# Optimization experiments

Measured on AMD Instinct MI355X. Metric: run time of the kernel, lower is better.

The kernel has to match this reference:

```python
import jax, jax.numpy as jnp
import numpy as np

D_MODEL = 1024
H = 16
D_K = D_MODEL // H
NEG_INF = -1.0e9  # matches masked_fill value in the torch source


def setup_inputs() -> dict:
    key = jax.random.key(0)
    kq, kk, kv, kwq, kwk, kwv, kwo = jax.random.split(key, 7)
    B, S = 2, 2048
    query = jax.random.normal(kq, (B, S, D_MODEL), dtype=jnp.float32)
    key_t = jax.random.normal(kk, (B, S, D_MODEL), dtype=jnp.float32)
    value = jax.random.normal(kv, (B, S, D_MODEL), dtype=jnp.float32)
    # causal mask: 1 = attend, 0 = masked (masked_fill(mask == 0, -1e9))
    masked_val = jnp.tril(jnp.ones((S, S), dtype=jnp.int32))[None, None, :, :]
    scale = 1.0 / np.sqrt(D_MODEL)
    w_q = jax.random.normal(kwq, (D_MODEL, D_MODEL), dtype=jnp.float32) * scale
    w_k = jax.random.normal(kwk, (D_MODEL, D_MODEL), dtype=jnp.float32) * scale
    w_v = jax.random.normal(kwv, (D_MODEL, D_MODEL), dtype=jnp.float32) * scale
    w_o = jax.random.normal(kwo, (D_MODEL, D_MODEL), dtype=jnp.float32) * scale
    return {"query": query, "key": key_t, "value": value, "masked_val": masked_val,
            "w_q": w_q, "w_k": w_k, "w_v": w_v, "w_o": w_o}


def reference(query, key, value, masked_val, w_q, w_k, w_v, w_o):
    B, Sq, _ = query.shape
    Sk = key.shape[1]
    # nn.Linear(x) = x @ W.T; weights stored as [out, in]
    Q = (query @ w_q.T).reshape(B, Sq, H, D_K).transpose(0, 2, 1, 3)  # [B,H,Sq,Dk]
    K = (key @ w_k.T).reshape(B, Sk, H, D_K).transpose(0, 2, 1, 3)    # [B,H,Sk,Dk]
    V = (value @ w_v.T).reshape(B, Sk, H, D_K).transpose(0, 2, 1, 3)  # [B,H,Sk,Dk]
    scores = jnp.einsum("bhqd,bhkd->bhqk", Q, K) / jnp.sqrt(jnp.float32(D_K))
    scores = jnp.where(masked_val == 0, NEG_INF, scores)
    probs = jax.nn.softmax(scores, axis=-1)  # dropout p=0.0 -> identity
    ctx = jnp.einsum("bhqk,bhkd->bhqd", probs, V)  # [B,H,Sq,Dk]
    ctx = ctx.transpose(0, 2, 1, 3).reshape(B, Sq, H * D_K)
    return ctx @ w_o.T
```

## Files before the change

### kernel.cpp

```cpp
#include <hip/hip_runtime.h>
#include <hip/hip_bf16.h>
#include <type_traits>

using bf16x8_t = __attribute__((ext_vector_type(8))) __bf16;
using f32x4_t  = __attribute__((ext_vector_type(4))) float;

#define MFMA16(a, b, c) __builtin_amdgcn_mfma_f32_16x16x32_bf16((a), (b), (c), 0, 0, 0)

constexpr int BATCH   = 2;
constexpr int SEQ     = 2048;
constexpr int DMODEL  = 1024;
constexpr int DK      = 64;
constexpr int MTOT    = BATCH * SEQ;
constexpr float SCL2 = 0.125f * 1.44269504088896f;

typedef const __attribute__((address_space(1))) unsigned int ga_u32;
typedef __attribute__((address_space(3))) unsigned int ls_u32;
__device__ __forceinline__ void glds16(const void* g, void* l) {
    __builtin_amdgcn_global_load_lds((ga_u32*)g, (ls_u32*)l, 16, 0, 0);
}

__device__ __forceinline__ float exp2_fast(float x) {
    float r;
    asm volatile("v_exp_f32 %0, %1" : "=v"(r) : "v"(x));
    return r;
}

__device__ __forceinline__ bf16x8_t cvt8(const float* __restrict__ p) {
    f32x4_t a = *(const f32x4_t*)p;
    f32x4_t b = *(const f32x4_t*)(p + 4);
    bf16x8_t r;
    r[0] = (__bf16)a[0]; r[1] = (__bf16)a[1]; r[2] = (__bf16)a[2]; r[3] = (__bf16)a[3];
    r[4] = (__bf16)b[0]; r[5] = (__bf16)b[1]; r[6] = (__bf16)b[2]; r[7] = (__bf16)b[3];
    return r;
}

__global__ __launch_bounds__(256) void cvt_all_kernel(
    const float* __restrict__ q, const float* __restrict__ k, const float* __restrict__ v,
    const float* __restrict__ w0, const float* __restrict__ w1,
    const float* __restrict__ w2, const float* __restrict__ w3,
    __bf16* __restrict__ dstA, __bf16* __restrict__ dstW)
{
    const int y = blockIdx.y;
    const float* src;
    __bf16* dst;
    if (y < 3) {
        const float* a[3] = {q, k, v};
        src = a[y];
        dst = dstA + (size_t)y * (MTOT * DMODEL);
    } else {
        if (blockIdx.x >= 512) return;
        const float* w[4] = {w0, w1, w2, w3};
        src = w[y - 3];
        dst = dstW + (size_t)(y - 3) * (DMODEL * DMODEL);
    }
    size_t i = ((size_t)blockIdx.x * 256 + threadIdx.x) * 8;
    *(bf16x8_t*)(dst + i) = cvt8(src + i);
}

template<bool C_F32>
__device__ __forceinline__ void gemm_body(
    const __bf16* __restrict__ A, const __bf16* __restrict__ Bt,
    void* __restrict__ Cp, int m0, int n0, float cscale)
{
    constexpr int K = DMODEL, N = DMODEL;
    constexpr int NS = K / 32;
    __shared__ __align__(16) char smem[3][16384];

    const int tid  = threadIdx.x;
    const int wave = tid >> 6, lane = tid & 63;
    const int wm = wave >> 1, wn = wave & 1;
    const int l15 = lane & 15, lhi = lane >> 4;

    auto stage = [&](int k0, int buf) {
        #pragma unroll
        for (int i = 0; i < 2; ++i) {
            int cbase = i * 256 + wave * 64;
            int slot = cbase + lane;
            int row = slot >> 2, c = slot & 3;
            int cs = (c + 4 - ((row >> 1) & 3)) & 3;
            glds16(A + (size_t)(m0 + row) * K + k0 + cs * 8, smem[buf] + (size_t)cbase * 16);
        }
        #pragma unroll
        for (int i = 0; i < 2; ++i) {
            int cbase = i * 256 + wave * 64;
            int slot = cbase + lane;
            int row = slot >> 2, c = slot & 3;
            int cs = (c + 4 - ((row >> 1) & 3)) & 3;
            glds16(Bt + (size_t)(n0 + row) * K + k0 + cs * 8,
                   smem[buf] + 8192 + (size_t)cbase * 16);
        }
    };

    f32x4_t acc[4][4] = {};

    auto mfma_step = [&](int buf) {
        const __bf16* a_ls = (const __bf16*)smem[buf];
        const __bf16* b_ls = (const __bf16*)(smem[buf] + 8192);
        bf16x8_t af[4], bfr[4];
        #pragma unroll
        for (int i = 0; i < 4; ++i) {
            int row = wm * 64 + i * 16 + l15;
            int lc = (lhi + (row >> 1)) & 3;
            af[i] = *(const bf16x8_t*)(a_ls + row * 32 + lc * 8);
        }
        #pragma unroll
        for (int j = 0; j < 4; ++j) {
            int row = wn * 64 + j * 16 + l15;
            int lc = (lhi + (row >> 1)) & 3;
            bfr[j] = *(const bf16x8_t*)(b_ls + row * 32 + lc * 8);
        }
        #pragma unroll
        for (int i = 0; i < 4; ++i)
            #pragma unroll
            for (int j = 0; j < 4; ++j)
                acc[i][j] = MFMA16(af[i], bfr[j], acc[i][j]);
    };

    stage(0, 0);
    stage(32, 1);

    for (int t = 0; t < NS - 2; ++t) {
        asm volatile("s_waitcnt vmcnt(4)" ::: "memory");
        __builtin_amdgcn_s_barrier();
        __builtin_amdgcn_sched_barrier(0);
        stage((t + 2) * 32, (t + 2) % 3);
        mfma_step(t % 3);
    }
    asm volatile("s_waitcnt vmcnt(4)" ::: "memory");
    __builtin_amdgcn_s_barrier();
    __builtin_amdgcn_sched_barrier(0);
    mfma_step((NS - 2) % 3);
    asm volatile("s_waitcnt vmcnt(0)" ::: "memory");
    __builtin_amdgcn_s_barrier();
    __builtin_amdgcn_sched_barrier(0);
    mfma_step((NS - 1) % 3);

    #pragma unroll
    for (int i = 0; i < 4; ++i)
        #pragma unroll
        for (int j = 0; j < 4; ++j)
            #pragma unroll
            for (int r = 0; r < 4; ++r) {
                int row = m0 + wm * 64 + i * 16 + lhi * 4 + r;
                int col = n0 + wn * 64 + j * 16 + l15;
                float v = acc[i][j][r] * cscale;
                if constexpr (C_F32)
                    ((float*)Cp)[(size_t)row * N + col] = v;
                else
                    ((__bf16*)Cp)[(size_t)row * N + col] = (__bf16)v;
            }
}

__global__ __launch_bounds__(256) void proj_qkv_kernel(
    const __bf16* __restrict__ act, const __bf16* __restrict__ wc,
    __bf16* __restrict__ oq, __bf16* __restrict__ ok, __bf16* __restrict__ ov)
{
    int lid = blockIdx.x + 8 * blockIdx.y + 256 * blockIdx.z;
    int nid = (lid & 7) * 96 + (lid >> 3);
    int z = nid >> 8, rem = nid & 255;
    int m0 = (rem >> 3) * 128, n0 = (rem & 7) * 128;

    const __bf16* A = act + (size_t)z * (MTOT * DMODEL);
    const __bf16* Bt = wc + (size_t)z * (DMODEL * DMODEL);
    __bf16* C; float cs;
    if (z == 0)      { C = oq; cs = SCL2; }
    else if (z == 1) { C = ok; cs = 1.0f; }
    else             { C = ov; cs = 1.0f; }
    gemm_body<false>(A, Bt, C, m0, n0, cs);
}

__global__ __launch_bounds__(256) void proj_out_kernel(
    const __bf16* __restrict__ ctx, const __bf16* __restrict__ woc, float* __restrict__ out)
{
    int lid = blockIdx.x + 8 * blockIdx.y;
    int nid = (lid & 7) * 32 + (lid >> 3);
    gemm_body<true>(ctx, woc, out, (nid >> 3) * 128, (nid & 7) * 128, 1.0f);
}

__global__ __launch_bounds__(512, 2) void attn_kernel(
    const __bf16* __restrict__ Qm, const __bf16* __restrict__ Km,
    const __bf16* __restrict__ Vm, __bf16* __restrict__ Om)
{
    constexpr int LDV = 72, LDP = 72;
    __shared__ __bf16 k_sh[2][64 * 64];
    __shared__ __bf16 v_sh[2][64 * LDV];
    __shared__ __bf16 p_sh[8][16 * LDP];

    const int tid  = threadIdx.x;
    const int wave = tid >> 6, lane = tid & 63;
    const int l15 = lane & 15, lhi = lane >> 4;

    int old = blockIdx.x + 16 * blockIdx.y;
    int nid = (old & 7) * 64 + (old >> 3);
    const int bh = nid >> 4, x = nid & 15;
    const int p = ((bh >> 1) & 1) ? 15 - x : x;
    const int q0 = p * 128;
    const int b = bh >> 4, h = bh & 15;

    const __bf16* Qb = Qm + (size_t)b * SEQ * DMODEL + h * DK;
    const __bf16* Kb = Km + (size_t)b * SEQ * DMODEL + h * DK;
    const __bf16* Vb = Vm + (size_t)b * SEQ * DMODEL + h * DK;

    const int qbase = q0 + wave * 16;

    bf16x8_t qf[2];
    {
        const __bf16* qp = Qb + (size_t)(qbase + l15) * DMODEL + lhi * 8;
        qf[0] = *(const bf16x8_t*)qp;
        qf[1] = *(const bf16x8_t*)(qp + 32);
    }
    bf16x8_t onesf;
    #pragma unroll
    for (int j = 0; j < 8; ++j) onesf[j] = (__bf16)1.0f;

    f32x4_t acc[4] = {};
    f32x4_t acc_l = {};

    const int vrow = tid >> 3, vgrp = tid & 7;
    bf16x8_t vreg;

    auto stageK = [&](int kv0, int buf) {
        int row = tid >> 3, c = (tid & 7) ^ (row & 7);
        glds16(Kb + (size_t)(kv0 + row) * DMODEL + c * 8,
               (char*)k_sh[buf] + (size_t)tid * 16);
    };
    auto loadV = [&](int kv0) {
        vreg = *(const bf16x8_t*)(Vb + (size_t)(kv0 + vrow) * DMODEL + vgrp * 8);
    };
    auto writeV = [&](int buf) {
        int sh = (vrow + vgrp * 8) & 63;
        #pragma unroll
        for (int j = 0; j < 8; ++j) v_sh[buf][(vgrp * 8 + j) * LDV + sh] = vreg[j];
    };

    auto body = [&](auto needmask_c, int kv0, int cur) {
        constexpr bool NEEDMASK = decltype(needmask_c)::value;
        const __bf16* ks_buf = k_sh[cur];
        const __bf16* vs_buf = v_sh[cur];

        f32x4_t sf[4] = {};
        __builtin_amdgcn_s_setprio(1);
        #pragma unroll
        for (int ks = 0; ks < 2; ++ks)
            #pragma unroll
            for (int n = 0; n < 4; ++n) {
                int row = n * 16 + l15;
                bf16x8_t kf = *(const bf16x8_t*)(ks_buf + row * 64 + (((ks * 4 + lhi) ^ (row & 7)) * 8));
                sf[n] = MFMA16(qf[ks], kf, sf[n]);
            }
        __builtin_amdgcn_s_setprio(0);

        const int qrow_base = qbase + lhi * 4;
        #pragma unroll
        for (int r = 0; r < 4; ++r)
            #pragma unroll
            for (int n = 0; n < 4; ++n) {
                float sv = sf[n][r];
                if constexpr (NEEDMASK)
                    if (kv0 + n * 16 + l15 > qrow_base + r) sv = -1.0e30f;
                p_sh[wave][(lhi * 4 + r) * LDP + ((n * 16 + l15 + ((lhi >> 1) << 3)) & 63)]
                    = (__bf16)exp2_fast(sv);
            }

        __builtin_amdgcn_s_setprio(1);
        #pragma unroll
        for (int ks = 0; ks < 2; ++ks) {
            bf16x8_t pa = *(const bf16x8_t*)(
                &p_sh[wave][l15 * LDP + ((ks * 32 + lhi * 8 + ((l15 >> 3) << 3)) & 63)]);
            acc_l = MFMA16(pa, onesf, acc_l);
            #pragma unroll
            for (int n = 0; n < 4; ++n) {
                int d = n * 16 + l15;
                int rot = (ks * 32 + lhi * 8 + ((d >> 3) << 3)) & 63;
                bf16x8_t vf = *(const bf16x8_t*)(vs_buf + d * LDV + rot);
                acc[n] = MFMA16(pa, vf, acc[n]);
            }
        }
        __builtin_amdgcn_s_setprio(0);
    };

    stageK(0, 0);
    loadV(0);
    writeV(0);
    __syncthreads();

    for (int t = 0; t < 2 * p; ++t) {
        stageK((t + 1) * 64, (t & 1) ^ 1);
        loadV((t + 1) * 64);
        body(std::integral_constant<bool, false>{}, t * 64, t & 1);
        writeV((t & 1) ^ 1);
        __syncthreads();
    }
    {
        const int t = 2 * p;
        stageK((t + 1) * 64, (t & 1) ^ 1);
        loadV((t + 1) * 64);
        body(std::integral_constant<bool, true>{}, t * 64, t & 1);
        writeV((t & 1) ^ 1);
        __syncthreads();
        body(std::integral_constant<bool, true>{}, (t + 1) * 64, (t + 1) & 1);
    }

    __bf16* Ob = Om + (size_t)b * SEQ * DMODEL + h * DK;
    #pragma unroll
    for (int n = 0; n < 4; ++n)
        #pragma unroll
        for (int r = 0; r < 4; ++r) {
            int row = qbase + lhi * 4 + r;
            Ob[(size_t)row * DMODEL + n * 16 + l15] = (__bf16)(acc[n][r] / acc_l[r]);
        }
}

extern "C" void kernel_launch(void* const* d_in, const int* in_sizes, int n_in,
                              void* d_out, int out_size, void* d_ws, size_t ws_size,
                              hipStream_t stream)
{
    const float* q  = (const float*)d_in[0];
    const float* k  = (const float*)d_in[1];
    const float* v  = (const float*)d_in[2];
    const float* wq = (const float*)d_in[4];
    const float* wk = (const float*)d_in[5];
    const float* wv = (const float*)d_in[6];
    const float* wo = (const float*)d_in[7];
    float* out = (float*)d_out;

    const size_t mat = (size_t)MTOT * DMODEL;
    __bf16* Qw = (__bf16*)d_ws;
    __bf16* Kw = Qw + mat;
    __bf16* Vw = Kw + mat;
    __bf16* Cw = Vw + mat;
    __bf16* Wc = Cw + mat;
    __bf16* Aw = Wc + 4 * (size_t)(DMODEL * DMODEL);

    dim3 blk(256);
    cvt_all_kernel<<<dim3(2048, 7), blk, 0, stream>>>(q, k, v, wq, wk, wv, wo, Aw, Wc);
    proj_qkv_kernel<<<dim3(8, 32, 3), blk, 0, stream>>>(Aw, Wc, Qw, Kw, Vw);
    attn_kernel<<<dim3(16, 32), dim3(512), 0, stream>>>(Qw, Kw, Vw, Cw);
    proj_out_kernel<<<dim3(8, 32), blk, 0, stream>>>(Cw, Wc + 3 * DMODEL * DMODEL, out);
}
```

Baseline: 110.4 us.

## Halve attention query tile to 64 rows with 4-wave blocks

The attention kernel now processes 64 query rows per block with 256 threads instead of 128 rows with 512 threads, doubling the grid. K/V staging is split so each thread loads two slots per tile. The causal loop now ends with a single masked diagonal tile, and the pairing/reversal of tile indices is adjusted for balance. This aims at finer load balancing and higher occupancy, at the cost of more K/V global traffic per query row.

```diff
diff --git a/kernel.cpp b/kernel.cpp
--- a/kernel.cpp
+++ b/kernel.cpp
@@ -178,24 +178,24 @@
     gemm_body<true>(ctx, woc, out, (nid >> 3) * 128, (nid & 7) * 128, 1.0f);
 }
 
-__global__ __launch_bounds__(512, 2) void attn_kernel(
+__global__ __launch_bounds__(256, 3) void attn_kernel(
     const __bf16* __restrict__ Qm, const __bf16* __restrict__ Km,
     const __bf16* __restrict__ Vm, __bf16* __restrict__ Om)
 {
     constexpr int LDV = 72, LDP = 72;
     __shared__ __bf16 k_sh[2][64 * 64];
     __shared__ __bf16 v_sh[2][64 * LDV];
-    __shared__ __bf16 p_sh[8][16 * LDP];
+    __shared__ __bf16 p_sh[4][16 * LDP];
 
     const int tid  = threadIdx.x;
     const int wave = tid >> 6, lane = tid & 63;
     const int l15 = lane & 15, lhi = lane >> 4;
 
-    int old = blockIdx.x + 16 * blockIdx.y;
-    int nid = (old & 7) * 64 + (old >> 3);
-    const int bh = nid >> 4, x = nid & 15;
-    const int p = ((bh >> 1) & 1) ? 15 - x : x;
-    const int q0 = p * 128;
+    int old = blockIdx.x + 32 * blockIdx.y;
+    int nid = (old & 7) * 128 + (old >> 3);
+    const int x = nid & 31, bh = nid >> 5;
+    const int p = (bh & 1) ? 31 - x : x;
+    const int q0 = p * 64;
     const int b = bh >> 4, h = bh & 15;
 
     const __bf16* Qb = Qm + (size_t)b * SEQ * DMODEL + h * DK;
@@ -218,20 +218,28 @@
     f32x4_t acc_l = {};
 
     const int vrow = tid >> 3, vgrp = tid & 7;
-    bf16x8_t vreg;
+    bf16x8_t vreg0, vreg1;
 
     auto stageK = [&](int kv0, int buf) {
-        int row = tid >> 3, c = (tid & 7) ^ (row & 7);
-        glds16(Kb + (size_t)(kv0 + row) * DMODEL + c * 8,
-               (char*)k_sh[buf] + (size_t)tid * 16);
+        #pragma unroll
+        for (int i = 0; i < 2; ++i) {
+            int slot = tid + i * 256;
+            int row = slot >> 3, c = (slot & 7) ^ (row & 7);
+            glds16(Kb + (size_t)(kv0 + row) * DMODEL + c * 8,
+                   (char*)k_sh[buf] + (size_t)slot * 16);
+        }
     };
     auto loadV = [&](int kv0) {
-        vreg = *(const bf16x8_t*)(Vb + (size_t)(kv0 + vrow) * DMODEL + vgrp * 8);
+        vreg0 = *(const bf16x8_t*)(Vb + (size_t)(kv0 + vrow) * DMODEL + vgrp * 8);
+        vreg1 = *(const bf16x8_t*)(Vb + (size_t)(kv0 + 32 + vrow) * DMODEL + vgrp * 8);
     };
     auto writeV = [&](int buf) {
-        int sh = (vrow + vgrp * 8) & 63;
-        #pragma unroll
-        for (int j = 0; j < 8; ++j) v_sh[buf][(vgrp * 8 + j) * LDV + sh] = vreg[j];
+        int sh0 = (vrow + vgrp * 8) & 63;
+        #pragma unroll
+        for (int j = 0; j < 8; ++j) v_sh[buf][(vgrp * 8 + j) * LDV + sh0] = vreg0[j];
+        int sh1 = (vrow + 32 + vgrp * 8) & 63;
+        #pragma unroll
+        for (int j = 0; j < 8; ++j) v_sh[buf][(vgrp * 8 + j) * LDV + sh1] = vreg1[j];
     };
 
     auto body = [&](auto needmask_c, int kv0, int cur) {
@@ -285,22 +293,14 @@
     writeV(0);
     __syncthreads();
 
-    for (int t = 0; t < 2 * p; ++t) {
+    for (int t = 0; t < p; ++t) {
         stageK((t + 1) * 64, (t & 1) ^ 1);
         loadV((t + 1) * 64);
         body(std::integral_constant<bool, false>{}, t * 64, t & 1);
         writeV((t & 1) ^ 1);
         __syncthreads();
     }
-    {
-        const int t = 2 * p;
-        stageK((t + 1) * 64, (t & 1) ^ 1);
-        loadV((t + 1) * 64);
-        body(std::integral_constant<bool, true>{}, t * 64, t & 1);
-        writeV((t & 1) ^ 1);
-        __syncthreads();
-        body(std::integral_constant<bool, true>{}, (t + 1) * 64, (t + 1) & 1);
-    }
+    body(std::integral_constant<bool, true>{}, p * 64, p & 1);
 
     __bf16* Ob = Om + (size_t)b * SEQ * DMODEL + h * DK;
     #pragma unroll
@@ -336,6 +336,6 @@
     dim3 blk(256);
     cvt_all_kernel<<<dim3(2048, 7), blk, 0, stream>>>(q, k, v, wq, wk, wv, wo, Aw, Wc);
     proj_qkv_kernel<<<dim3(8, 32, 3), blk, 0, stream>>>(Aw, Wc, Qw, Kw, Vw);
-    attn_kernel<<<dim3(16, 32), dim3(512), 0, stream>>>(Qw, Kw, Vw, Cw);
+    attn_kernel<<<dim3(32, 32), blk, 0, stream>>>(Qw, Kw, Vw, Cw);
     proj_out_kernel<<<dim3(8, 32), blk, 0, stream>>>(Cw, Wc + 3 * DMODEL * DMODEL, out);
 }
```

New measurement: 117.3 us. +6.2%, slower.

## Split attention KV range across two blocks and merge partials in separate kernel

Applied to the files above, without the earlier changes.

Each query tile's causal KV range is split into two halves processed by separate blocks, doubling the attention grid to improve load balance and CU occupancy. Unnormalized partial outputs and row sums are written to workspace, and a new merge kernel sums them and normalizes into the context buffer. There is no running max, so merging needs only a sum, because scores are exponentiated directly. The cost is an extra kernel launch and extra global traffic for the partials.

```diff
diff --git a/kernel.cpp b/kernel.cpp
--- a/kernel.cpp
+++ b/kernel.cpp
@@ -180,7 +180,7 @@
 
 __global__ __launch_bounds__(512, 2) void attn_kernel(
     const __bf16* __restrict__ Qm, const __bf16* __restrict__ Km,
-    const __bf16* __restrict__ Vm, __bf16* __restrict__ Om)
+    const __bf16* __restrict__ Vm, __bf16* __restrict__ pa, float* __restrict__ pl)
 {
     constexpr int LDV = 72, LDP = 72;
     __shared__ __bf16 k_sh[2][64 * 64];
@@ -191,10 +191,11 @@
     const int wave = tid >> 6, lane = tid & 63;
     const int l15 = lane & 15, lhi = lane >> 4;
 
-    int old = blockIdx.x + 16 * blockIdx.y;
-    int nid = (old & 7) * 64 + (old >> 3);
-    const int bh = nid >> 4, x = nid & 15;
-    const int p = ((bh >> 1) & 1) ? 15 - x : x;
+    int old = blockIdx.x + 32 * blockIdx.y;
+    int nid = (old & 7) * 128 + (old >> 3);
+    const int x5 = nid & 31, bh = nid >> 5;
+    const int praw = x5 >> 1, s = x5 & 1;
+    const int p = (bh & 1) ? 15 - praw : praw;
     const int q0 = p * 128;
     const int b = bh >> 4, h = bh & 15;
 
@@ -266,50 +267,79 @@
         __builtin_amdgcn_s_setprio(1);
         #pragma unroll
         for (int ks = 0; ks < 2; ++ks) {
-            bf16x8_t pa = *(const bf16x8_t*)(
+            bf16x8_t pa_f = *(const bf16x8_t*)(
                 &p_sh[wave][l15 * LDP + ((ks * 32 + lhi * 8 + ((l15 >> 3) << 3)) & 63)]);
-            acc_l = MFMA16(pa, onesf, acc_l);
+            acc_l = MFMA16(pa_f, onesf, acc_l);
             #pragma unroll
             for (int n = 0; n < 4; ++n) {
                 int d = n * 16 + l15;
                 int rot = (ks * 32 + lhi * 8 + ((d >> 3) << 3)) & 63;
                 bf16x8_t vf = *(const bf16x8_t*)(vs_buf + d * LDV + rot);
-                acc[n] = MFMA16(pa, vf, acc[n]);
+                acc[n] = MFMA16(pa_f, vf, acc[n]);
             }
         }
         __builtin_amdgcn_s_setprio(0);
     };
 
-    stageK(0, 0);
-    loadV(0);
-    writeV(0);
+    const int tstart = s ? (p + 1) : 0;
+    const int tend   = s ? (2 * p + 2) : (p + 1);
+    const int tm     = s ? tstart : p;
+
+    stageK(tstart * 64, tstart & 1);
+    loadV(tstart * 64);
+    writeV(tstart & 1);
     __syncthreads();
 
-    for (int t = 0; t < 2 * p; ++t) {
+    for (int t = tstart; t < tm; ++t) {
         stageK((t + 1) * 64, (t & 1) ^ 1);
         loadV((t + 1) * 64);
         body(std::integral_constant<bool, false>{}, t * 64, t & 1);
         writeV((t & 1) ^ 1);
         __syncthreads();
     }
-    {
-        const int t = 2 * p;
-        stageK((t + 1) * 64, (t & 1) ^ 1);
-        loadV((t + 1) * 64);
+    for (int t = tm; t < tend; ++t) {
+        int nx = (t + 1 < tend) ? (t + 1) : t;
+        stageK(nx * 64, (t & 1) ^ 1);
+        loadV(nx * 64);
         body(std::integral_constant<bool, true>{}, t * 64, t & 1);
         writeV((t & 1) ^ 1);
         __syncthreads();
-        body(std::integral_constant<bool, true>{}, (t + 1) * 64, (t + 1) & 1);
-    }
-
-    __bf16* Ob = Om + (size_t)b * SEQ * DMODEL + h * DK;
+    }
+
+    const size_t rbase = (size_t)(s * 32 + bh) * SEQ;
     #pragma unroll
     for (int n = 0; n < 4; ++n)
         #pragma unroll
         for (int r = 0; r < 4; ++r) {
             int row = qbase + lhi * 4 + r;
-            Ob[(size_t)row * DMODEL + n * 16 + l15] = (__bf16)(acc[n][r] / acc_l[r]);
-        }
+            pa[(rbase + row) * 64 + n * 16 + l15] = (__bf16)acc[n][r];
+        }
+    if (l15 == 0) {
+        #pragma unroll
+        for (int r = 0; r < 4; ++r)
+            pl[rbase + qbase + lhi * 4 + r] = acc_l[r];
+    }
+}
+
+__global__ __launch_bounds__(256) void attn_merge_kernel(
+    const __bf16* __restrict__ pa, const float* __restrict__ pl, __bf16* __restrict__ Cw)
+{
+    size_t i = (size_t)blockIdx.x * 256 + threadIdx.x;
+    size_t rowg = i >> 3;
+    int d0 = (int)(i & 7) * 8;
+    int bh = (int)(rowg >> 11);
+    int row = (int)(rowg & 2047);
+    int b = bh >> 4, h = bh & 15;
+
+    float l0 = pl[rowg], l1 = pl[(size_t)32 * SEQ + rowg];
+    float inv = 1.0f / (l0 + l1);
+    bf16x8_t a0 = *(const bf16x8_t*)(pa + rowg * 64 + d0);
+    bf16x8_t a1 = *(const bf16x8_t*)(pa + (size_t)32 * SEQ * 64 + rowg * 64 + d0);
+    bf16x8_t o;
+    #pragma unroll
+    for (int j = 0; j < 8; ++j)
+        o[j] = (__bf16)(((float)a0[j] + (float)a1[j]) * inv);
+    *(bf16x8_t*)(Cw + ((size_t)b * SEQ + row) * DMODEL + h * DK + d0) = o;
 }
 
 extern "C" void kernel_launch(void* const* d_in, const int* in_sizes, int n_in,
@@ -332,10 +362,13 @@
     __bf16* Cw = Vw + mat;
     __bf16* Wc = Cw + mat;
     __bf16* Aw = Wc + 4 * (size_t)(DMODEL * DMODEL);
+    __bf16* Pa = Aw;
+    float*  Pl = (float*)(Aw + 2 * mat);
 
     dim3 blk(256);
     cvt_all_kernel<<<dim3(2048, 7), blk, 0, stream>>>(q, k, v, wq, wk, wv, wo, Aw, Wc);
     proj_qkv_kernel<<<dim3(8, 32, 3), blk, 0, stream>>>(Aw, Wc, Qw, Kw, Vw);
-    attn_kernel<<<dim3(16, 32), dim3(512), 0, stream>>>(Qw, Kw, Vw, Cw);
+    attn_kernel<<<dim3(32, 32), dim3(512), 0, stream>>>(Qw, Kw, Vw, Pa, Pl);
+    attn_merge_kernel<<<dim3(2048), blk, 0, stream>>>(Pa, Pl, Cw);
     proj_out_kernel<<<dim3(8, 32), blk, 0, stream>>>(Cw, Wc + 3 * DMODEL * DMODEL, out);
 }
```

Measured after the change: 114.2 us. 1.03x slower.
